# Optimization experiments

Hardware: AMD Instinct MI355X
Metric: run time of the kernel (lower is better)

Reference implementation:

```python
import jax, jax.numpy as jnp
import numpy as np
import math

B, S, H, NH = 2, 1024, 768, 12
DH = H // NH  # 64

def setup_inputs() -> dict:
    key = jax.random.key(0)
    ks = jax.random.split(key, 8)
    sc = 0.02
    return {
        "hidden_states": jax.random.normal(ks[0], (B, S, H), jnp.float32),
        "bbox_pos_emb": jax.random.normal(ks[1], (S, S, B, DH), jnp.float32),
        "attention_mask": jnp.zeros((B, 1, 1, S), jnp.float32),
        "Wq": jax.random.normal(ks[2], (H, H), jnp.float32) * sc,
        "bq": jnp.zeros((H,), jnp.float32),
        "Wk": jax.random.normal(ks[3], (H, H), jnp.float32) * sc,
        "bk": jnp.zeros((H,), jnp.float32),
        "Wv": jax.random.normal(ks[4], (H, H), jnp.float32) * sc,
        "bv": jnp.zeros((H,), jnp.float32),
    }

def reference(hidden_states, bbox_pos_emb, attention_mask, Wq, bq, Wk, bk, Wv, bv):
    b, s, h = hidden_states.shape
    def proj(W, bias):
        # (b, s, h) -> (b, nh, s, dh)
        y = hidden_states @ W.T + bias
        return y.reshape(b, s, NH, DH).transpose(0, 2, 1, 3)
    q = proj(Wq, bq)
    k = proj(Wk, bk)
    v = proj(Wv, bv)
    # QK^T: (b, nh, s, s)
    scores = jnp.einsum("bnid,bnjd->bnij", q, k)
    # bbox bias: (s, s, b, dh) -> (b, s, s, dh); bnid,bijd->bnij
    bbox = bbox_pos_emb.transpose(2, 0, 1, 3)
    scores = scores + jnp.einsum("bnid,bijd->bnij", q, bbox)
    scores = scores / math.sqrt(DH)
    scores = scores + attention_mask
    probs = jax.nn.softmax(scores, axis=-1)
    ctx = jnp.einsum("bnij,bnjd->bnid", probs, v)
    ctx = ctx.transpose(0, 2, 1, 3).reshape(b, s, h)
    return ctx
```

## Files before the change

kernel.cpp:

```cpp
#include <hip/hip_runtime.h>
#include <hip/hip_bf16.h>

typedef short bf4 __attribute__((ext_vector_type(4)));
typedef short short8 __attribute__((ext_vector_type(8)));
typedef float f32x4 __attribute__((ext_vector_type(4)));

#define MFMA(a, b, c) __builtin_amdgcn_mfma_f32_16x16x32_bf16((a), (b), (c), 0, 0, 0)

#define NB 2
#define NS 1024
#define NHID 768
#define NHEAD 12
#define NDH 64

__device__ __forceinline__ short f2bf(float x) {
    __hip_bfloat16 h = __float2bfloat16(x);
    return *reinterpret_cast<short*>(&h);
}

__device__ __forceinline__ int xcd_swz(int orig, int nwg) {
    return (orig & 7) * (nwg >> 3) + (orig >> 3);
}

typedef const __attribute__((address_space(1))) void gas_t;
typedef __attribute__((address_space(3))) void las_t;
__device__ __forceinline__ void gld_lds16(const float* g, float* l) {
    __builtin_amdgcn_global_load_lds((gas_t*)g, (las_t*)l, 16, 0, 0);
}
__device__ __forceinline__ void gld_lds16s(const short* g, short* l) {
    __builtin_amdgcn_global_load_lds((gas_t*)g, (las_t*)l, 16, 0, 0);
}

#define NHE (2048 * 768)
#define WE  (768 * 768)
__global__ void cvt_bf16_all(
    const float* __restrict__ hidden,
    const float* __restrict__ Wq, const float* __restrict__ Wk,
    const float* __restrict__ Wv,
    short* __restrict__ Xbf, short* __restrict__ Wbf)
{
    const int base = (blockIdx.x * 256 + threadIdx.x) * 4;
    const float* src; short* dst; int off;
    if (base < NHE)               { src = hidden; dst = Xbf;          off = base; }
    else if (base < NHE + WE)     { src = Wq;     dst = Wbf;          off = base - NHE; }
    else if (base < NHE + 2 * WE) { src = Wk;     dst = Wbf + WE;     off = base - NHE - WE; }
    else                          { src = Wv;     dst = Wbf + 2 * WE; off = base - NHE - 2 * WE; }
    f32x4 v = *reinterpret_cast<const f32x4*>(src + off);
    bf4 r;
    r[0] = f2bf(v[0]); r[1] = f2bf(v[1]); r[2] = f2bf(v[2]); r[3] = f2bf(v[3]);
    *reinterpret_cast<bf4*>(dst + off) = r;
}

__global__ __launch_bounds__(256, 3) void qkv_gemm(
    const short* __restrict__ Xbf, const short* __restrict__ Wbf,
    const float* __restrict__ bq, const float* __restrict__ bk,
    const float* __restrict__ bv,
    short* __restrict__ Qo, short* __restrict__ Ko, short* __restrict__ VTo)
{
    const int lane = threadIdx.x & 63;
    const int wave = threadIdx.x >> 6;
    const int lg = lane >> 4, lr = lane & 15;

    const int wgid = xcd_swz(blockIdx.x, 16 * 36);
    const int m0 = (wgid / 36) * 128;
    const int n0 = (wgid % 36) * 64;
    const int proj = n0 / NHID;
    const int ncol0 = n0 % NHID;
    const float* bias = proj == 0 ? bq : (proj == 1 ? bk : bv);

    __shared__ short Alds[2][128 * 64];
    __shared__ short Blds[2][64 * 64];

    f32x4 acc[2][4];
    #pragma unroll
    for (int mm = 0; mm < 2; ++mm)
        #pragma unroll
        for (int s = 0; s < 4; ++s) acc[mm][s] = (f32x4){0.f, 0.f, 0.f, 0.f};

    auto stage = [&](int t, int buf) {
        const int k0 = t * 64;
        #pragma unroll
        for (int p = 0; p < 4; ++p) {
            const int op = wave * 4 + p;
            const int unit = op * 64 + lane;
            const int r = unit >> 3, u = unit & 7;
            const int g = u ^ (r & 7);
            gld_lds16s(Xbf + (size_t)(m0 + r) * NHID + k0 + g * 8,
                       &Alds[buf][op * 512]);
        }
        #pragma unroll
        for (int p = 0; p < 2; ++p) {
            const int op = wave * 2 + p;
            const int unit = op * 64 + lane;
            const int r = unit >> 3, u = unit & 7;
            const int g = u ^ (r & 7);
            gld_lds16s(Wbf + (size_t)(n0 + r) * NHID + k0 + g * 8,
                       &Blds[buf][op * 512]);
        }
    };

    auto compute = [&](int buf) {
        #pragma unroll
        for (int kk = 0; kk < 2; ++kk) {
            const int U = kk * 4 + lg;
            short8 a[2];
            #pragma unroll
            for (int mm = 0; mm < 2; ++mm) {
                const int R = wave * 32 + mm * 16 + lr;
                a[mm] = *reinterpret_cast<const short8*>(
                    &Alds[buf][(R * 8 + (U ^ (R & 7))) * 8]);
            }
            #pragma unroll
            for (int s = 0; s < 4; ++s) {
                const int R = s * 16 + lr;
                short8 b = *reinterpret_cast<const short8*>(
                    &Blds[buf][(R * 8 + (U ^ (R & 7))) * 8]);
                acc[0][s] = MFMA(a[0], b, acc[0][s]);
                acc[1][s] = MFMA(a[1], b, acc[1][s]);
            }
        }
    };

    stage(0, 0);
    #pragma unroll 2
    for (int t = 0; t < 12; ++t) {
        const int buf = t & 1;
        asm volatile("s_waitcnt vmcnt(0)" ::: "memory");
        __syncthreads();
        if (t < 11) stage(t + 1, buf ^ 1);
        compute(buf);
    }

    #pragma unroll
    for (int mm = 0; mm < 2; ++mm) {
        #pragma unroll
        for (int s = 0; s < 4; ++s) {
            const int ncol = ncol0 + s * 16 + lr;
            const float badd = bias[ncol];
            #pragma unroll
            for (int r = 0; r < 4; ++r) {
                const int m = m0 + wave * 32 + mm * 16 + lg * 4 + r;
                const short v16 = f2bf(acc[mm][s][r] + badd);
                if (proj == 0) {
                    Qo[(size_t)m * NHID + ncol] = v16;
                } else if (proj == 1) {
                    Ko[(size_t)m * NHID + ncol] = v16;
                } else {
                    const int b = m >> 10, ss = m & 1023;
                    const int h = ncol >> 6, dd = ncol & 63;
                    VTo[(((size_t)(b * NHEAD + h) * NDH + dd) << 10) + ss] = v16;
                }
            }
        }
    }
}

__global__ __launch_bounds__(256, 2) void bias_gemm(
    const short* __restrict__ Q,
    const float* __restrict__ bbox,
    const float* __restrict__ mask,
    short* __restrict__ biasH)
{
    const int lane = threadIdx.x & 63;
    const int wave = threadIdx.x >> 6;
    const int lg = lane >> 4, lr = lane & 15;
    const int i = blockIdx.x;
    const int jq = wave * 256;

    __shared__ float lds[4][2][2048];

    short8 qa[2][2];
    #pragma unroll
    for (int b2 = 0; b2 < 2; ++b2)
        #pragma unroll
        for (int kk = 0; kk < 2; ++kk)
            qa[b2][kk] = *reinterpret_cast<const short8*>(
                Q + ((size_t)(b2 * NS) + i) * NHID + lr * 64 + kk * 32 + lg * 8);

    const int r_half = lane >> 5;
    const int u_lin = lane & 31;

    auto stage = [&](int t, int buf) {
        const int j0 = jq + t * 16;
        float* dst = &lds[wave][buf][0];
        #pragma unroll
        for (int w = 0; w < 8; ++w) {
            const int r = 2 * w + r_half;
            const int u = u_lin ^ (r & 7);
            const float* src = bbox + (size_t)(i * NS + j0 + r) * 128 + u * 4;
            gld_lds16(src, dst + w * 256);
        }
    };

    auto compute = [&](int t, int buf) {
        const float* tile = &lds[wave][buf][0];
        const int j0 = jq + t * 16;
        const int x = lr & 7;
        #pragma unroll
        for (int b2 = 0; b2 < 2; ++b2) {
            const float mk = mask[b2 * NS + j0 + lr];
            f32x4 c = (f32x4){0.f, 0.f, 0.f, 0.f};
            #pragma unroll
            for (int kk = 0; kk < 2; ++kk) {
                const int q0 = b2 * 16 + kk * 8 + lg * 2;
                f32x4 ca = *reinterpret_cast<const f32x4*>(tile + (size_t)(lr * 32 + ((q0)     ^ x)) * 4);
                f32x4 cb = *reinterpret_cast<const f32x4*>(tile + (size_t)(lr * 32 + ((q0 + 1) ^ x)) * 4);
                short8 bf;
                bf[0] = f2bf(ca[0]); bf[1] = f2bf(ca[1]); bf[2] = f2bf(ca[2]); bf[3] = f2bf(ca[3]);
                bf[4] = f2bf(cb[0]); bf[5] = f2bf(cb[1]); bf[6] = f2bf(cb[2]); bf[7] = f2bf(cb[3]);
                c = MFMA(qa[b2][kk], bf, c);
            }
            if (lg < 3) {
                #pragma unroll
                for (int r = 0; r < 4; ++r) {
                    const int n = lg * 4 + r;
                    biasH[((size_t)(b2 * NHEAD + n) * NS + i) * NS + j0 + lr] =
                        f2bf(c[r] * 0.125f + mk);
                }
            }
        }
    };

    stage(0, 0);
    for (int t = 0; t < 16; ++t) {
        const int buf = t & 1;
        asm volatile("s_waitcnt lgkmcnt(0)" ::: "memory");
        if (t < 15) stage(t + 1, buf ^ 1);
        if (t == 0 || t == 15) asm volatile("s_waitcnt vmcnt(8)"  ::: "memory");
        else                   asm volatile("s_waitcnt vmcnt(16)" ::: "memory");
        compute(t, buf);
    }
}

__global__ __launch_bounds__(256, 3) void attn3(
    const short* __restrict__ Q,
    const short* __restrict__ K,
    const short* __restrict__ VT,
    const short* __restrict__ biasH,
    float* __restrict__ out)
{
    const int tid = threadIdx.x;
    const int lane = tid & 63;
    const int wave = tid >> 6;
    const int lg = lane >> 4, lr = lane & 15;

    const int wgid = xcd_swz(blockIdx.x, 24 * 16);
    const int bh = wgid >> 4;
    const int ic = wgid & 15;
    const int b = bh / NHEAD, h = bh % NHEAD;
    const int i0 = ic * 64 + wave * 16;

    __shared__ short Klds[2][2048];
    __shared__ short Vlds[2][2048];
    __shared__ short Blds[2][2048];
    __shared__ short plds[4][16 * 40];

    short8 qa[2];
    #pragma unroll
    for (int kk = 0; kk < 2; ++kk)
        qa[kk] = *reinterpret_cast<const short8*>(
            Q + ((size_t)(b * NS) + i0 + lr) * NHID + h * 64 + kk * 32 + lg * 8);

    const short* Kb = K + (size_t)b * NS * NHID + h * 64;
    const short* Vb = VT + (size_t)(b * NHEAD + h) * NDH * NS;
    const short* Bb = biasH + ((size_t)(b * NHEAD + h) * NS + ic * 64) * NS;

    f32x4 ctx[4];
    #pragma unroll
    for (int dt = 0; dt < 4; ++dt) ctx[dt] = (f32x4){0.f, 0.f, 0.f, 0.f};
    f32x4 den = (f32x4){0.f, 0.f, 0.f, 0.f};

    const int kr = tid >> 3, ku = tid & 7;
    const int kgu = ku ^ (kr & 7);
    const int vr = tid >> 2, vu = tid & 3;
    const int vgu = vu ^ (vr & 3);
    const int br = tid >> 2, bu = tid & 3;

    auto stage = [&](int t, int buf) {
        const int j0 = t * 32;
        gld_lds16s(Kb + (size_t)(j0 + kr) * NHID + kgu * 8, &Klds[buf][tid * 8]);
        gld_lds16s(Vb + (size_t)vr * NS + j0 + vgu * 8,     &Vlds[buf][tid * 8]);
        gld_lds16s(Bb + (size_t)br * NS + j0 + bu * 8,      &Blds[buf][tid * 8]);
    };

    auto compute = [&](int buf) {
        f32x4 sc[2];
        #pragma unroll
        for (int s = 0; s < 2; ++s) {
            f32x4 c = (f32x4){0.f, 0.f, 0.f, 0.f};
            #pragma unroll
            for (int kk = 0; kk < 2; ++kk) {
                const int R = s * 16 + lr;
                const int U = kk * 4 + lg;
                short8 kf = *reinterpret_cast<const short8*>(
                    &Klds[buf][(R * 8 + (U ^ (R & 7))) * 8]);
                c = MFMA(qa[kk], kf, c);
            }
            sc[s] = c;
        }
        #pragma unroll
        for (int s = 0; s < 2; ++s)
            #pragma unroll
            for (int r = 0; r < 4; ++r) {
                const unsigned int u = (unsigned int)(unsigned short)
                    Blds[buf][wave * 512 + (lg * 4 + r) * 32 + s * 16 + lr] << 16;
                float bb;
                __builtin_memcpy(&bb, &u, 4);
                sc[s][r] = __expf(sc[s][r] * 0.125f + bb);
            }
        den += sc[0] + sc[1];

        #pragma unroll
        for (int s = 0; s < 2; ++s)
            #pragma unroll
            for (int r = 0; r < 4; ++r)
                plds[wave][(lg * 4 + r) * 40 + s * 16 + lr] = f2bf(sc[s][r]);
        asm volatile("" ::: "memory");
        short8 pa = *reinterpret_cast<const short8*>(&plds[wave][lr * 40 + lg * 8]);
        asm volatile("" ::: "memory");

        #pragma unroll
        for (int dt = 0; dt < 4; ++dt) {
            const int R = dt * 16 + lr;
            short8 vf = *reinterpret_cast<const short8*>(
                &Vlds[buf][(R * 4 + (lg ^ (R & 3))) * 8]);
            ctx[dt] = MFMA(pa, vf, ctx[dt]);
        }
    };

    stage(0, 0);
    for (int t = 0; t < 32; ++t) {
        const int buf = t & 1;
        asm volatile("s_waitcnt vmcnt(0)" ::: "memory");
        __syncthreads();
        if (t < 31) stage(t + 1, buf ^ 1);
        compute(buf);
    }

    #pragma unroll
    for (int w = 1; w < 16; w <<= 1) {
        f32x4 o;
        #pragma unroll
        for (int r = 0; r < 4; ++r) o[r] = __shfl_xor(den[r], w, 64);
        den += o;
    }

    #pragma unroll
    for (int r = 0; r < 4; ++r) {
        const float inv = 1.0f / den[r];
        const int i = i0 + lg * 4 + r;
        #pragma unroll
        for (int dt = 0; dt < 4; ++dt)
            out[((size_t)(b * NS) + i) * NHID + h * 64 + dt * 16 + lr] =
                ctx[dt][r] * inv;
    }
}

extern "C" void kernel_launch(void* const* d_in, const int* in_sizes, int n_in,
                              void* d_out, int out_size, void* d_ws, size_t ws_size,
                              hipStream_t stream) {
    (void)in_sizes; (void)n_in; (void)out_size; (void)ws_size;
    const float* hidden = (const float*)d_in[0];
    const float* bbox   = (const float*)d_in[1];
    const float* mask   = (const float*)d_in[2];
    const float* Wq = (const float*)d_in[3]; const float* bq = (const float*)d_in[4];
    const float* Wk = (const float*)d_in[5]; const float* bk = (const float*)d_in[6];
    const float* Wv = (const float*)d_in[7]; const float* bv = (const float*)d_in[8];
    float* out = (float*)d_out;

    char* ws = (char*)d_ws;
    const size_t qkv_bytes = (size_t)NB * NS * NHID * sizeof(short);
    short* Qw  = (short*)ws;
    short* Kw  = (short*)(ws + qkv_bytes);
    short* VTw = (short*)(ws + 2 * qkv_bytes);
    short* biasH = (short*)(ws + 3 * qkv_bytes);
    const size_t bias_bytes = (size_t)NB * NHEAD * NS * NS * sizeof(short);
    short* Xbf = (short*)(ws + 3 * qkv_bytes + bias_bytes);
    short* Wbf = Xbf + (size_t)2048 * NHID;

    const int cvt_total = (NHE + 3 * WE) / 4;
    cvt_bf16_all<<<cvt_total / 256, 256, 0, stream>>>(hidden, Wq, Wk, Wv, Xbf, Wbf);

    qkv_gemm<<<16 * 36, 256, 0, stream>>>(Xbf, Wbf, bq, bk, bv, Qw, Kw, VTw);

    bias_gemm<<<NS, 256, 0, stream>>>(Qw, bbox, mask, biasH);

    attn3<<<24 * 16, 256, 0, stream>>>(Qw, Kw, VTw, biasH, out);
}
```

Before: 215.7 us.

## Triple-buffer LDS pipelines and shrink QKV GEMM M-tile to 64

The QKV GEMM tile height drops from 128 to 64 rows, doubling the grid to 1152 workgroups and cutting per-wave accumulators. Both the GEMM and the attention kernel move from double to triple LDS buffering. The next stage is now issued before a partial vmcnt wait, so one tile load stays in flight while the current tile is computed. The intent is to hide global-load latency and add parallelism. In exchange, each A tile gets less reuse and the kernels use more LDS, and the partial-wait counts must match the number of loads issued per stage.

```diff
diff --git a/kernel.cpp b/kernel.cpp
--- a/kernel.cpp
+++ b/kernel.cpp
@@ -61,27 +61,25 @@
     const int wave = threadIdx.x >> 6;
     const int lg = lane >> 4, lr = lane & 15;
 
-    const int wgid = xcd_swz(blockIdx.x, 16 * 36);
-    const int m0 = (wgid / 36) * 128;
+    const int wgid = xcd_swz(blockIdx.x, 32 * 36);
+    const int m0 = (wgid / 36) * 64;
     const int n0 = (wgid % 36) * 64;
     const int proj = n0 / NHID;
     const int ncol0 = n0 % NHID;
     const float* bias = proj == 0 ? bq : (proj == 1 ? bk : bv);
 
-    __shared__ short Alds[2][128 * 64];
-    __shared__ short Blds[2][64 * 64];
-
-    f32x4 acc[2][4];
-    #pragma unroll
-    for (int mm = 0; mm < 2; ++mm)
-        #pragma unroll
-        for (int s = 0; s < 4; ++s) acc[mm][s] = (f32x4){0.f, 0.f, 0.f, 0.f};
+    __shared__ short Alds[3][64 * 64];
+    __shared__ short Blds[3][64 * 64];
+
+    f32x4 acc[4];
+    #pragma unroll
+    for (int s = 0; s < 4; ++s) acc[s] = (f32x4){0.f, 0.f, 0.f, 0.f};
 
     auto stage = [&](int t, int buf) {
         const int k0 = t * 64;
         #pragma unroll
-        for (int p = 0; p < 4; ++p) {
-            const int op = wave * 4 + p;
+        for (int p = 0; p < 2; ++p) {
+            const int op = wave * 2 + p;
             const int unit = op * 64 + lane;
             const int r = unit >> 3, u = unit & 7;
             const int g = u ^ (r & 7);
@@ -103,53 +101,47 @@
         #pragma unroll
         for (int kk = 0; kk < 2; ++kk) {
             const int U = kk * 4 + lg;
-            short8 a[2];
-            #pragma unroll
-            for (int mm = 0; mm < 2; ++mm) {
-                const int R = wave * 32 + mm * 16 + lr;
-                a[mm] = *reinterpret_cast<const short8*>(
-                    &Alds[buf][(R * 8 + (U ^ (R & 7))) * 8]);
-            }
+            const int Ra = wave * 16 + lr;
+            short8 a = *reinterpret_cast<const short8*>(
+                &Alds[buf][(Ra * 8 + (U ^ (Ra & 7))) * 8]);
             #pragma unroll
             for (int s = 0; s < 4; ++s) {
                 const int R = s * 16 + lr;
                 short8 b = *reinterpret_cast<const short8*>(
                     &Blds[buf][(R * 8 + (U ^ (R & 7))) * 8]);
-                acc[0][s] = MFMA(a[0], b, acc[0][s]);
-                acc[1][s] = MFMA(a[1], b, acc[1][s]);
+                acc[s] = MFMA(a, b, acc[s]);
             }
         }
     };
 
     stage(0, 0);
-    #pragma unroll 2
     for (int t = 0; t < 12; ++t) {
-        const int buf = t & 1;
-        asm volatile("s_waitcnt vmcnt(0)" ::: "memory");
-        __syncthreads();
-        if (t < 11) stage(t + 1, buf ^ 1);
-        compute(buf);
-    }
-
-    #pragma unroll
-    for (int mm = 0; mm < 2; ++mm) {
-        #pragma unroll
-        for (int s = 0; s < 4; ++s) {
-            const int ncol = ncol0 + s * 16 + lr;
-            const float badd = bias[ncol];
-            #pragma unroll
-            for (int r = 0; r < 4; ++r) {
-                const int m = m0 + wave * 32 + mm * 16 + lg * 4 + r;
-                const short v16 = f2bf(acc[mm][s][r] + badd);
-                if (proj == 0) {
-                    Qo[(size_t)m * NHID + ncol] = v16;
-                } else if (proj == 1) {
-                    Ko[(size_t)m * NHID + ncol] = v16;
-                } else {
-                    const int b = m >> 10, ss = m & 1023;
-                    const int h = ncol >> 6, dd = ncol & 63;
-                    VTo[(((size_t)(b * NHEAD + h) * NDH + dd) << 10) + ss] = v16;
-                }
+        if (t < 11) {
+            stage(t + 1, (t + 1) % 3);
+            asm volatile("s_waitcnt vmcnt(4)" ::: "memory");
+        } else {
+            asm volatile("s_waitcnt vmcnt(0)" ::: "memory");
+        }
+        __builtin_amdgcn_s_barrier();
+        compute(t % 3);
+    }
+
+    #pragma unroll
+    for (int s = 0; s < 4; ++s) {
+        const int ncol = ncol0 + s * 16 + lr;
+        const float badd = bias[ncol];
+        #pragma unroll
+        for (int r = 0; r < 4; ++r) {
+            const int m = m0 + wave * 16 + lg * 4 + r;
+            const short v16 = f2bf(acc[s][r] + badd);
+            if (proj == 0) {
+                Qo[(size_t)m * NHID + ncol] = v16;
+            } else if (proj == 1) {
+                Ko[(size_t)m * NHID + ncol] = v16;
+            } else {
+                const int b = m >> 10, ss = m & 1023;
+                const int h = ncol >> 6, dd = ncol & 63;
+                VTo[(((size_t)(b * NHEAD + h) * NDH + dd) << 10) + ss] = v16;
             }
         }
     }
@@ -250,9 +242,9 @@
     const int b = bh / NHEAD, h = bh % NHEAD;
     const int i0 = ic * 64 + wave * 16;
 
-    __shared__ short Klds[2][2048];
-    __shared__ short Vlds[2][2048];
-    __shared__ short Blds[2][2048];
+    __shared__ short Klds[3][2048];
+    __shared__ short Vlds[3][2048];
+    __shared__ short Blds[3][2048];
     __shared__ short plds[4][16 * 40];
 
     short8 qa[2];
@@ -330,11 +322,14 @@
 
     stage(0, 0);
     for (int t = 0; t < 32; ++t) {
-        const int buf = t & 1;
-        asm volatile("s_waitcnt vmcnt(0)" ::: "memory");
-        __syncthreads();
-        if (t < 31) stage(t + 1, buf ^ 1);
-        compute(buf);
+        if (t < 31) {
+            stage(t + 1, (t + 1) % 3);
+            asm volatile("s_waitcnt vmcnt(3)" ::: "memory");
+        } else {
+            asm volatile("s_waitcnt vmcnt(0)" ::: "memory");
+        }
+        __builtin_amdgcn_s_barrier();
+        compute(t % 3);
     }
 
     #pragma unroll
@@ -381,7 +376,7 @@
     const int cvt_total = (NHE + 3 * WE) / 4;
     cvt_bf16_all<<<cvt_total / 256, 256, 0, stream>>>(hidden, Wq, Wk, Wv, Xbf, Wbf);
 
-    qkv_gemm<<<16 * 36, 256, 0, stream>>>(Xbf, Wbf, bq, bk, bv, Qw, Kw, VTw);
+    qkv_gemm<<<32 * 36, 256, 0, stream>>>(Xbf, Wbf, bq, bk, bv, Qw, Kw, VTw);
 
     bias_gemm<<<NS, 256, 0, stream>>>(Qw, bbox, mask, biasH);
 
```

Result: faster. 207.9 us (-3.6%).
